# Kernel tuning notes

Hardware: AMD Instinct MI355X
Metric: run time of the kernel (lower is better)

Reference implementation:

```python
import jax, jax.numpy as jnp
import numpy as np

B, G, A, NC, NL = 64, 32, 25600, 2, 5
IOU_T, RATIO, FACE = 0.5, 3, 1
A_BOX, A_LMK, A_GAZE = 1.0, 0.5, 1.0
VAR_C, VAR_S = 0.1, 0.2  # SSD encode variances


def cxcywh_to_xyxy(b):
    return jnp.concatenate([b[..., :2] - b[..., 2:] / 2, b[..., :2] + b[..., 2:] / 2], -1)


def make_anchors():
    g = 160  # 160*160 = 25600 anchors
    c = (jnp.arange(g, dtype=jnp.float32) + 0.5) / g
    cy, cx = jnp.meshgrid(c, c, indexing='ij')
    wh = jnp.full((g * g, 2), 0.04, jnp.float32)
    return jnp.concatenate([cx.reshape(-1, 1), cy.reshape(-1, 1), wh], 1)  # [A,4] cxcywh


def setup_inputs() -> dict:
    key = jax.random.key(0)
    ks = jax.random.split(key, 8)
    cxy = jax.random.uniform(ks[0], (B, G, 2), minval=0.1, maxval=0.9)
    wh = jax.random.uniform(ks[1], (B, G, 2), minval=0.03, maxval=0.25)
    gt_boxes = jnp.concatenate([cxy - wh / 2, cxy + wh / 2], -1)  # xyxy in [0,1]
    return {
        'cls_logits': jax.random.normal(ks[2], (B, A, NC)),
        'box_preds': jax.random.normal(ks[3], (B, A, 4)),
        'lmk_preds': jax.random.normal(ks[4], (B, A, NL * 2)),
        'gaze_preds': jax.random.normal(ks[5], (B, A, 2)),
        'anchors': make_anchors(),
        'gt_boxes': gt_boxes,
        'gt_labels': jax.random.randint(ks[6], (B, G), 0, 2, jnp.int32),  # 0=pad, 1=face
        'gt_landmarks': jax.random.uniform(ks[7], (B, G, NL * 2)),
        'gt_gaze': jax.random.normal(jax.random.fold_in(key, 9), (B, G, 2)) * 0.3,
    }


def _smooth_l1(x):
    ax = jnp.abs(x)
    return jnp.where(ax < 1.0, 0.5 * ax * ax, ax - 0.5)


def _iou(gt, anc):  # [G,4],[A,4] xyxy -> [G,A]
    tl = jnp.maximum(gt[:, None, :2], anc[None, :, :2])
    br = jnp.minimum(gt[:, None, 2:], anc[None, :, 2:])
    inter = jnp.prod(jnp.clip(br - tl, 0.0), -1)
    ag = jnp.prod(gt[:, 2:] - gt[:, :2], -1)
    aa = jnp.prod(anc[:, 2:] - anc[:, :2], -1)
    return inter / (ag[:, None] + aa[None, :] - inter + 1e-9)


def _build_targets(anchors, gt_boxes, gt_labels, gt_landmarks, gt_gaze):
    anchors_xyxy = cxcywh_to_xyxy(anchors)
    dcxy, dwh = anchors[:, :2], anchors[:, 2:]

    def match(gt_b, lab, lmk, gz):
        valid = lab > 0
        iou = jnp.where(valid[:, None], _iou(gt_b, anchors_xyxy), -1.0)  # [G,A]
        # each valid GT claims its best anchor
        best_anchor_idx = jnp.where(valid, jnp.argmax(iou, 1), A)  # A -> dropped
        matches = jnp.full((A,), -1, jnp.int32).at[best_anchor_idx].set(
            jnp.arange(G, dtype=jnp.int32), mode='drop')
        # anchors above IoU threshold take their best GT
        best_gt_iou = iou.max(0)
        best_gt_idx = jnp.argmax(iou, 0).astype(jnp.int32)
        matches = jnp.where(best_gt_iou >= IOU_T, best_gt_idx, matches)
        pos = matches >= 0
        m = jnp.clip(matches, 0)
        cls = jnp.where(pos, lab[m], 0)
        g = gt_b[m]  # [A,4] xyxy
        gcxy = (g[:, :2] + g[:, 2:]) / 2
        gwh = g[:, 2:] - g[:, :2]
        off = jnp.concatenate([(gcxy - dcxy) / dwh / VAR_C,
                               jnp.log(jnp.clip(gwh / dwh, 1e-6)) / VAR_S], -1)
        off = jnp.where(pos[:, None], off, 0.0)
        face = (cls == FACE) & pos
        lm = lmk[m].reshape(A, NL, 2)
        lmo = ((lm - dcxy[:, None, :]) / dwh[:, None, :] / VAR_C).reshape(A, NL * 2)
        lmo = jnp.where(face[:, None], lmo, 0.0)
        gzt = jnp.where(face[:, None], gz[m], 0.0)
        return cls, off, lmo, gzt

    return jax.vmap(match)(gt_boxes, gt_labels, gt_landmarks, gt_gaze)


def reference(cls_logits, box_preds, lmk_preds, gaze_preds, anchors,
              gt_boxes, gt_labels, gt_landmarks, gt_gaze):
    cls_t, box_t, lmk_t, gaze_t = _build_targets(anchors, gt_boxes, gt_labels,
                                                 gt_landmarks, gt_gaze)
    pos = cls_t > 0  # [B,A]
    num_pos = jnp.maximum(pos.sum(1), 1)  # [B] int
    npos_f = num_pos.sum().astype(jnp.float32)

    logp = jax.nn.log_softmax(cls_logits, -1)
    cls_loss = -jnp.take_along_axis(logp, cls_t[..., None], -1)[..., 0]  # [B,A]
    pos_sum = jnp.where(pos, cls_loss, 0.0).sum()
    # hard negative mining: per-image top-k of negative CE losses
    neg_losses = jnp.where(pos, -jnp.inf, cls_loss)
    srt = jnp.sort(neg_losses, 1)[:, ::-1]
    num_neg = jnp.minimum((~pos).sum(1), RATIO * num_pos)  # [B]
    take = jnp.arange(A)[None, :] < num_neg[:, None]
    neg_sum = jnp.where(take, srt, 0.0).sum()
    total_cls = (pos_sum + neg_sum) / npos_f

    total_box = jnp.where(pos[..., None], _smooth_l1(box_preds - box_t), 0.0).sum() / npos_f

    face = (cls_t == FACE) & pos
    nface_f = jnp.maximum(face.sum(1), 1).sum().astype(jnp.float32)
    total_lmk = jnp.where(face[..., None], _smooth_l1(lmk_preds - lmk_t), 0.0).sum() / nface_f
    total_gaze = jnp.where(face[..., None], _smooth_l1(gaze_preds - gaze_t), 0.0).sum() / nface_f

    total = total_cls + A_BOX * total_box + A_LMK * total_lmk + A_GAZE * total_gaze
    return (total, total_cls, total_box, total_lmk, total_gaze)
```

## Files before the change

### kernel.cpp

```cpp
#include <hip/hip_runtime.h>
#include <stdint.h>

#define B 64
#define G 32
#define A 25600
#define NC 2
#define NL 5
#define IOU_T 0.5f
#define VAR_C 0.1f
#define VAR_S 0.2f

#define MSPLIT 50
#define MCH (A / MSPLIT)
#define PF 8

#define NB2 256
#define BSCALE2 20.0f
#define CANDCAP 8192
#define ST 512
#define NW (ST / 64)

__device__ __forceinline__ float sl1(float x) {
    float ax = fabsf(x);
    return ax < 1.0f ? 0.5f * ax * ax : ax - 0.5f;
}

__device__ __forceinline__ int vbin(float closs) {
    int bin = (int)(closs * BSCALE2);
    return bin < 0 ? 0 : (bin > NB2 - 1 ? NB2 - 1 : bin);
}

__global__ __launch_bounds__(256) void fused_kernel(
    const float* __restrict__ cls_logits, const float* __restrict__ box_preds,
    const float* __restrict__ lmk_preds, const float* __restrict__ gaze_preds,
    const float* __restrict__ anchors, const float* __restrict__ gt_boxes,
    const int* __restrict__ gt_labels, const float* __restrict__ gt_lmk,
    const float* __restrict__ gt_gaze, signed char* __restrict__ matches,
    unsigned long long* __restrict__ gsplit, unsigned* __restrict__ negkey,
    unsigned* __restrict__ bhist, float* __restrict__ psplit,
    unsigned* __restrict__ gdone)
{
    const int b = blockIdx.x, s = blockIdx.y, tid = threadIdx.x;
    const int lane = tid & 63, wave = tid >> 6;
    __shared__ float4 sbox[G];
    __shared__ int sgorig[G], sinv[G];
    __shared__ unsigned long long sbest[G];
    __shared__ int s_nv;
    __shared__ float sgb[G * 4], slmk[G * NL * 2], sgz[G * 2];
    __shared__ int slab[G];
    __shared__ unsigned lhist[4][NB2];
    __shared__ float wred[4][8];

    if (b == 0 && s == 0 && tid == 0) *gdone = 0u;

    if (tid < G) {
        sbest[tid] = 0ULL;
        int valid = gt_labels[b * G + tid] > 0;
        unsigned long long mask = __ballot(valid);
        int pfx = __popcll(mask & ((1ULL << tid) - 1ULL));
        sinv[tid] = valid ? pfx : -1;
        if (valid) {
            sbox[pfx] = *(const float4*)(gt_boxes + (b * G + tid) * 4);
            sgorig[pfx] = tid;
        }
        if (tid == 0) s_nv = (int)__popcll(mask);
    }
    for (int i = tid; i < G * 4; i += 256) sgb[i] = gt_boxes[b * G * 4 + i];
    for (int i = tid; i < G * NL * 2; i += 256) slmk[i] = gt_lmk[b * G * NL * 2 + i];
    for (int i = tid; i < G * 2; i += 256) sgz[i] = gt_gaze[b * G * 2 + i];
    if (tid < G) slab[tid] = gt_labels[b * G + tid];
    for (int i = tid; i < 4 * NB2; i += 256) ((unsigned*)lhist)[i] = 0u;
    __syncthreads();
    const int nv = s_nv;

    signed char* mrow = matches + (size_t)b * A;
    const int a0 = s * MCH;
    const int aL = a0 + tid, aH = aL + 256;

    float4 anL = *(const float4*)(anchors + aL * 4);
    float4 anH = *(const float4*)(anchors + aH * 4);
    float axL0 = anL.x - anL.z * 0.5f, ayL0 = anL.y - anL.w * 0.5f;
    float axL1 = anL.x + anL.z * 0.5f, ayL1 = anL.y + anL.w * 0.5f;
    float aaL = (axL1 - axL0) * (ayL1 - ayL0);
    float axH0 = anH.x - anH.z * 0.5f, ayH0 = anH.y - anH.w * 0.5f;
    float axH1 = anH.x + anH.z * 0.5f, ayH1 = anH.y + anH.w * 0.5f;
    float aaH = (axH1 - axH0) * (ayH1 - ayH0);

    float wx0 = fminf(axL0, axH0), wy0 = fminf(ayL0, ayH0);
    float wx1 = fmaxf(axL1, axH1), wy1 = fmaxf(ayL1, ayH1);
    #pragma unroll
    for (int off = 32; off > 0; off >>= 1) {
        wx0 = fminf(wx0, __shfl_down(wx0, off));
        wy0 = fminf(wy0, __shfl_down(wy0, off));
        wx1 = fmaxf(wx1, __shfl_down(wx1, off));
        wy1 = fmaxf(wy1, __shfl_down(wy1, off));
    }
    wx0 = __shfl(wx0, 0); wy0 = __shfl(wy0, 0);
    wx1 = __shfl(wx1, 0); wy1 = __shfl(wy1, 0);

    float bestL = -2.0f, bestH = -2.0f;
    int bciL = 0, bciH = 0;
    for (int ci = 0; ci < nv; ++ci) {
        float4 bb = sbox[ci];
        if (bb.x < wx1 && bb.z > wx0 && bb.y < wy1 && bb.w > wy0) {
            float area = (bb.z - bb.x) * (bb.w - bb.y);
            float iwL = fmaxf(fminf(bb.z, axL1) - fmaxf(bb.x, axL0), 0.0f);
            float ihL = fmaxf(fminf(bb.w, ayL1) - fmaxf(bb.y, ayL0), 0.0f);
            float interL = iwL * ihL;
            float iwH = fmaxf(fminf(bb.z, axH1) - fmaxf(bb.x, axH0), 0.0f);
            float ihH = fmaxf(fminf(bb.w, ayH1) - fmaxf(bb.y, ayH0), 0.0f);
            float interH = iwH * ihH;
            float iouL = 0.0f, iouH = 0.0f;
            if (__any(interL > 0.0f || interH > 0.0f)) {
                iouL = interL / (area + aaL - interL + 1e-9f);
                iouH = interH / (area + aaH - interH + 1e-9f);
                unsigned long long keyL =
                    ((unsigned long long)__float_as_uint(iouL) << 32) |
                    (unsigned)(0xFFFFFFFFu - (unsigned)aL);
                unsigned long long keyH =
                    ((unsigned long long)__float_as_uint(iouH) << 32) |
                    (unsigned)(0xFFFFFFFFu - (unsigned)aH);
                unsigned long long km = keyL > keyH ? keyL : keyH;
                #pragma unroll
                for (int off = 32; off > 0; off >>= 1) {
                    unsigned long long o = __shfl_down(km, off);
                    if (o > km) km = o;
                }
                if (lane == 0 && km > sbest[ci]) atomicMax(&sbest[ci], km);
            }
            if (iouL > bestL) { bestL = iouL; bciL = ci; }
            if (iouH > bestH) { bestH = iouH; bciH = ci; }
        } else {
            if (bestL < 0.0f) { bestL = 0.0f; bciL = ci; }
            if (bestH < 0.0f) { bestH = 0.0f; bciH = ci; }
        }
    }
    const int vL = (bestL >= IOU_T) ? sgorig[bciL] : -1;
    const int vH = (bestH >= IOU_T) ? sgorig[bciH] : -1;
    mrow[aL] = (signed char)vL;
    mrow[aH] = (signed char)vH;

    const float* lrow = cls_logits + (size_t)b * A * NC;
    unsigned* krow = negkey + (size_t)b * A;

    float pos_sum = 0, box_sum = 0, lmk_sum = 0, gaze_sum = 0;
    float pos_cnt = 0, face_cnt = 0;

    #pragma unroll
    for (int h = 0; h < 2; ++h) {
        const int a = h ? aH : aL;
        const int v = h ? vH : vL;
        const float4 an = h ? anH : anL;
        float2 xl = *(const float2*)(lrow + a * 2);
        float x0 = xl.x, x1 = xl.y;
        float mx = fmaxf(x0, x1);
        float lse = mx + logf(expf(x0 - mx) + expf(x1 - mx));
        unsigned key = 0;
        if (v < 0) {
            float closs = lse - x0;
            unsigned bits = __float_as_uint(closs);
            key = bits ^ ((bits & 0x80000000u) ? 0xFFFFFFFFu : 0x80000000u);
            atomicAdd(&lhist[wave][vbin(closs)], 1u);
        } else {
            int m = v;
            int lab = slab[m];
            float xc = (lab >= 1) ? x1 : x0;
            pos_sum += lse - xc;
            pos_cnt += 1.0f;
            float dcx = an.x, dcy = an.y, dw = an.z, dh = an.w;
            float bx0 = sgb[m * 4], by0 = sgb[m * 4 + 1];
            float bx1 = sgb[m * 4 + 2], by1 = sgb[m * 4 + 3];
            float gcx = (bx0 + bx1) * 0.5f, gcy = (by0 + by1) * 0.5f;
            float gw = bx1 - bx0, gh = by1 - by0;
            float off0 = ((gcx - dcx) / dw) / VAR_C;
            float off1 = ((gcy - dcy) / dh) / VAR_C;
            float off2 = logf(fmaxf(gw / dw, 1e-6f)) / VAR_S;
            float off3 = logf(fmaxf(gh / dh, 1e-6f)) / VAR_S;
            float4 bp = *(const float4*)(box_preds + ((size_t)b * A + a) * 4);
            box_sum += sl1(bp.x - off0) + sl1(bp.y - off1) +
                       sl1(bp.z - off2) + sl1(bp.w - off3);
            if (lab == 1) {
                face_cnt += 1.0f;
                const float* lp = lmk_preds + ((size_t)b * A + a) * (NL * 2);
                #pragma unroll
                for (int i = 0; i < NL; ++i) {
                    float tx = ((slmk[m * NL * 2 + 2 * i] - dcx) / dw) / VAR_C;
                    float ty = ((slmk[m * NL * 2 + 2 * i + 1] - dcy) / dh) / VAR_C;
                    lmk_sum += sl1(lp[2 * i] - tx) + sl1(lp[2 * i + 1] - ty);
                }
                const float* gp = gaze_preds + ((size_t)b * A + a) * 2;
                gaze_sum += sl1(gp[0] - sgz[m * 2]) + sl1(gp[1] - sgz[m * 2 + 1]);
            }
        }
        krow[a] = key;
    }

    #pragma unroll
    for (int off = 32; off > 0; off >>= 1) {
        pos_sum += __shfl_down(pos_sum, off);
        box_sum += __shfl_down(box_sum, off);
        lmk_sum += __shfl_down(lmk_sum, off);
        gaze_sum += __shfl_down(gaze_sum, off);
        pos_cnt += __shfl_down(pos_cnt, off);
        face_cnt += __shfl_down(face_cnt, off);
    }
    if (lane == 0) {
        wred[wave][0] = pos_sum; wred[wave][1] = box_sum;
        wred[wave][2] = lmk_sum; wred[wave][3] = gaze_sum;
        wred[wave][4] = pos_cnt; wred[wave][5] = face_cnt;
    }
    __syncthreads();
    if (tid < 6) {
        psplit[(b * MSPLIT + s) * PF + tid] =
            wred[0][tid] + wred[1][tid] + wred[2][tid] + wred[3][tid];
    }
    bhist[(b * MSPLIT + s) * NB2 + tid] =
        lhist[0][tid] + lhist[1][tid] + lhist[2][tid] + lhist[3][tid];
    if (tid < G) {
        int ci = sinv[tid];
        gsplit[((size_t)b * MSPLIT + s) * G + tid] = (ci >= 0) ? sbest[ci] : 0ULL;
    }
}

__global__ __launch_bounds__(ST) void select_kernel(
    const float* __restrict__ cls_logits, const float* __restrict__ box_preds,
    const float* __restrict__ lmk_preds, const float* __restrict__ gaze_preds,
    const float* __restrict__ anchors, const float* __restrict__ gt_boxes,
    const int* __restrict__ gt_labels, const float* __restrict__ gt_lmk,
    const float* __restrict__ gt_gaze, const signed char* __restrict__ matches,
    const unsigned long long* __restrict__ gsplit,
    unsigned* __restrict__ negkey, const unsigned* __restrict__ bhist,
    const float* __restrict__ psplit, unsigned* __restrict__ candbuf,
    float* __restrict__ partials, unsigned* __restrict__ gdone,
    float* __restrict__ out)
{
    const int b = blockIdx.x, tid = threadIdx.x;
    const int lane = tid & 63, wv = tid >> 6;
    __shared__ unsigned lhist[NB2];
    __shared__ unsigned whist[NW][256];
    __shared__ float accs[8];
    __shared__ float swred[NW];
    __shared__ int s_t, s_fin;
    __shared__ unsigned s_kk, s_candN, s_pfx, s_k2;

    unsigned* krow = negkey + (size_t)b * A;
    const uint4* krow4 = (const uint4*)krow;
    const float* lrow = cls_logits + (size_t)b * A * NC;
    unsigned* cand = candbuf + (size_t)b * CANDCAP;

    if (tid < 6) {
        float v = 0;
        for (int s2 = 0; s2 < MSPLIT; ++s2) v += psplit[(b * MSPLIT + s2) * PF + tid];
        accs[tid] = v;
    }
    if (tid < NB2) {
        unsigned v = 0;
        const unsigned* hb = bhist + (size_t)b * MSPLIT * NB2 + tid;
        for (int s2 = 0; s2 < MSPLIT; ++s2) v += hb[s2 * NB2];
        lhist[tid] = v;
    }
    if (tid == 0) s_candN = 0;
    __syncthreads();

    float f0 = 0, f1 = 0, f2 = 0, f3 = 0, f4 = 0, f5 = 0;
    int fbin = -1, fa = -1;
    if (tid < 32) {
        const int g = tid;
        int lab = gt_labels[b * G + g];
        unsigned long long kb = 0ULL;
        const unsigned long long* gs = gsplit + (size_t)b * MSPLIT * G + g;
        for (int s2 = 0; s2 < MSPLIT; ++s2) {
            unsigned long long v = gs[(size_t)s2 * G];
            if (v > kb) kb = v;
        }
        int a_c = -1;
        if (lab > 0 && kb != 0ULL) {
            unsigned a = 0xFFFFFFFFu - (unsigned)(kb & 0xFFFFFFFFu);
            if (matches[(size_t)b * A + a] < 0) a_c = (int)a;
        }
        bool win = a_c >= 0;
        for (int j = 0; j < 32; ++j) {
            int aj = __shfl(a_c, j);
            if (j > g && a_c >= 0 && aj == a_c) win = false;
        }
        if (win) {
            const int a = a_c;
            float2 xl = *(const float2*)(lrow + a * 2);
            float x0 = xl.x, x1 = xl.y;
            float mx = fmaxf(x0, x1);
            float lse = mx + logf(expf(x0 - mx) + expf(x1 - mx));
            float xc = (lab >= 1) ? x1 : x0;
            f0 = lse - xc; f4 = 1.0f;
            float4 an = *(const float4*)(anchors + a * 4);
            const float* gb = gt_boxes + (b * G + g) * 4;
            float bx0 = gb[0], by0 = gb[1], bx1 = gb[2], by1 = gb[3];
            float gcx = (bx0 + bx1) * 0.5f, gcy = (by0 + by1) * 0.5f;
            float gw = bx1 - bx0, gh = by1 - by0;
            float off0 = ((gcx - an.x) / an.z) / VAR_C;
            float off1 = ((gcy - an.y) / an.w) / VAR_C;
            float off2 = logf(fmaxf(gw / an.z, 1e-6f)) / VAR_S;
            float off3 = logf(fmaxf(gh / an.w, 1e-6f)) / VAR_S;
            float4 bp = *(const float4*)(box_preds + ((size_t)b * A + a) * 4);
            f1 = sl1(bp.x - off0) + sl1(bp.y - off1) +
                 sl1(bp.z - off2) + sl1(bp.w - off3);
            if (lab == 1) {
                f5 = 1.0f;
                const float* gl = gt_lmk + (b * G + g) * NL * 2;
                const float* lp = lmk_preds + ((size_t)b * A + a) * (NL * 2);
                #pragma unroll
                for (int i = 0; i < NL; ++i) {
                    float tx = ((gl[2 * i] - an.x) / an.z) / VAR_C;
                    float ty = ((gl[2 * i + 1] - an.y) / an.w) / VAR_C;
                    f2 += sl1(lp[2 * i] - tx) + sl1(lp[2 * i + 1] - ty);
                }
                const float* gz = gt_gaze + (b * G + g) * 2;
                const float* gp = gaze_preds + ((size_t)b * A + a) * 2;
                f3 = sl1(gp[0] - gz[0]) + sl1(gp[1] - gz[1]);
            }
            unsigned key = krow[a];
            float closs = __uint_as_float(key ^ 0x80000000u);
            fbin = vbin(closs); fa = a;
        }
    }
    if (tid < 64) {
        #pragma unroll
        for (int off = 16; off > 0; off >>= 1) {
            f0 += __shfl_down(f0, off); f1 += __shfl_down(f1, off);
            f2 += __shfl_down(f2, off); f3 += __shfl_down(f3, off);
            f4 += __shfl_down(f4, off); f5 += __shfl_down(f5, off);
        }
        if (tid == 0) {
            accs[0] += f0; accs[1] += f1; accs[2] += f2;
            accs[3] += f3; accs[4] += f4; accs[5] += f5;
        }
    }
    if (fbin >= 0) {
        atomicSub(&lhist[fbin], 1u);
        krow[fa] = 0u;
    }
    __syncthreads();

    unsigned pos_t = (unsigned)accs[4];
    unsigned face_t = (unsigned)accs[5];
    unsigned num_pos = pos_t > 1u ? pos_t : 1u;
    unsigned neg_cnt = (unsigned)A - pos_t;
    unsigned k = 3u * num_pos; if (neg_cnt < k) k = neg_cnt;

    if (tid < 64) {
        unsigned c[4]; unsigned csum = 0;
        #pragma unroll
        for (int j = 0; j < 4; ++j) { c[j] = lhist[tid * 4 + j]; csum += c[j]; }
        unsigned S = csum;
        #pragma unroll
        for (int off = 1; off < 64; off <<= 1) {
            unsigned t2 = __shfl_down(S, off);
            if (tid + off < 64) S += t2;
        }
        unsigned excl = S - csum;
        if (excl < k && excl + csum >= k) {
            unsigned cum = excl;
            #pragma unroll
            for (int j = 3; j >= 0; --j) {
                unsigned h = c[j];
                if (cum + h >= k) { s_t = tid * 4 + j; s_kk = k - cum; break; }
                cum += h;
            }
        }
    }
    __syncthreads();
    const int t = s_t;
    const unsigned kk_bin = s_kk;

    float nsum_top = 0.0f;
    for (int i = tid; i < A / 4; i += ST) {
        uint4 kv = krow4[i];
        #pragma unroll
        for (int j = 0; j < 4; ++j) {
            unsigned key = (&kv.x)[j];
            bool cp = false;
            if (key != 0u) {
                float closs = __uint_as_float(key ^ 0x80000000u);
                int bin = vbin(closs);
                if (bin > t) nsum_top += closs;
                else if (bin == t) cp = true;
            }
            unsigned long long m = __ballot(cp);
            if (m != 0ULL) {
                int leader = __ffsll((long long)m) - 1;
                unsigned base = 0u;
                if (lane == leader)
                    base = atomicAdd(&s_candN, (unsigned)__popcll(m));
                base = __shfl(base, leader);
                if (cp) {
                    unsigned idx = base + (unsigned)__popcll(m & ((1ULL << lane) - 1ULL));
                    if (idx < CANDCAP) cand[idx] = key;
                }
            }
        }
    }
    __syncthreads();
    const unsigned candN = s_candN;
    const bool fast = candN <= CANDCAP;

    unsigned pfx = 0, kk = kk_bin;
    for (int p = 0; p < 4; ++p) {
        for (int i = tid; i < NW * 256; i += ST) ((unsigned*)whist)[i] = 0u;
        __syncthreads();
        const int shift = 24 - 8 * p;
        if (fast) {
            for (unsigned i = tid; i < candN; i += ST) {
                unsigned key = cand[i];
                if (p == 0 || (key >> (shift + 8)) == pfx)
                    atomicAdd(&whist[wv][(key >> shift) & 0xFFu], 1u);
            }
        } else {
            for (int a = tid; a < A; a += ST) {
                unsigned key = krow[a];
                if (key != 0u && vbin(__uint_as_float(key ^ 0x80000000u)) == t &&
                    (p == 0 || (key >> (shift + 8)) == pfx))
                    atomicAdd(&whist[wv][(key >> shift) & 0xFFu], 1u);
            }
        }
        __syncthreads();
        if (tid < 64) {
            unsigned c[4]; unsigned csum = 0;
            #pragma unroll
            for (int j = 0; j < 4; ++j) {
                unsigned v = 0;
                #pragma unroll
                for (int w = 0; w < NW; ++w) v += whist[w][tid * 4 + j];
                c[j] = v; csum += v;
            }
            unsigned S = csum;
            #pragma unroll
            for (int off = 1; off < 64; off <<= 1) {
                unsigned t2 = __shfl_down(S, off);
                if (tid + off < 64) S += t2;
            }
            unsigned excl = S - csum;
            if (excl < kk && excl + csum >= kk) {
                unsigned cum = excl;
                #pragma unroll
                for (int j = 3; j >= 0; --j) {
                    unsigned h = c[j];
                    if (cum + h >= kk) {
                        s_pfx = (pfx << 8) | (unsigned)(tid * 4 + j);
                        s_k2 = kk - cum;
                        break;
                    }
                    cum += h;
                }
            }
        }
        __syncthreads();
        pfx = s_pfx; kk = s_k2;
    }
    const unsigned Tkey = pfx;
    const unsigned krem = kk;
    const float Tval = __uint_as_float(Tkey ^ 0x80000000u);

    float csum2 = 0.0f;
    if (fast) {
        for (unsigned i = tid; i < candN; i += ST) {
            unsigned key = cand[i];
            if (key > Tkey) csum2 += __uint_as_float(key ^ 0x80000000u);
        }
    } else {
        for (int a = tid; a < A; a += ST) {
            unsigned key = krow[a];
            if (key != 0u) {
                float closs = __uint_as_float(key ^ 0x80000000u);
                if (vbin(closs) == t && key > Tkey) csum2 += closs;
            }
        }
    }
    float tot = nsum_top + csum2;
    #pragma unroll
    for (int off = 32; off > 0; off >>= 1) tot += __shfl_down(tot, off);
    if (lane == 0) swred[wv] = tot;
    __syncthreads();
    if (tid == 0) {
        float r = 0;
        #pragma unroll
        for (int w = 0; w < NW; ++w) r += swred[w];
        float* pr = partials + b * PF;
        pr[0] = accs[0]; pr[1] = accs[1]; pr[2] = accs[2]; pr[3] = accs[3];
        pr[4] = r + (float)krem * Tval;
        pr[5] = (float)num_pos;
        pr[6] = (float)(face_t > 1u ? face_t : 1u);
        __threadfence();
        unsigned r2 = atomicAdd(gdone, 1u);
        s_fin = (r2 == B - 1);
    }
    __syncthreads();
    if (!s_fin) return;
    __threadfence();

    if (tid < 64) {
        int tt = tid;
        float ps = partials[tt * PF + 0], bs = partials[tt * PF + 1];
        float ls = partials[tt * PF + 2], gs = partials[tt * PF + 3];
        float ns = partials[tt * PF + 4], npos = partials[tt * PF + 5];
        float nf = partials[tt * PF + 6];
        #pragma unroll
        for (int o = 32; o > 0; o >>= 1) {
            ps += __shfl_down(ps, o); bs += __shfl_down(bs, o);
            ls += __shfl_down(ls, o); gs += __shfl_down(gs, o);
            ns += __shfl_down(ns, o); npos += __shfl_down(npos, o);
            nf += __shfl_down(nf, o);
        }
        if (tt == 0) {
            float tc = (ps + ns) / npos;
            float tb = bs / npos;
            float tl = ls / nf;
            float tg = gs / nf;
            out[0] = tc + 1.0f * tb + 0.5f * tl + 1.0f * tg;
            out[1] = tc; out[2] = tb; out[3] = tl; out[4] = tg;
        }
    }
}

extern "C" void kernel_launch(void* const* d_in, const int* in_sizes, int n_in,
                              void* d_out, int out_size, void* d_ws, size_t ws_size,
                              hipStream_t stream) {
    const float* cls_logits = (const float*)d_in[0];
    const float* box_preds  = (const float*)d_in[1];
    const float* lmk_preds  = (const float*)d_in[2];
    const float* gaze_preds = (const float*)d_in[3];
    const float* anchors    = (const float*)d_in[4];
    const float* gt_boxes   = (const float*)d_in[5];
    const int*   gt_labels  = (const int*)d_in[6];
    const float* gt_lmk     = (const float*)d_in[7];
    const float* gt_gaze    = (const float*)d_in[8];

    char* ws = (char*)d_ws;
    signed char* matches = (signed char*)ws;             ws += (size_t)B * A;
    unsigned long long* gsplit = (unsigned long long*)ws; ws += (size_t)B * MSPLIT * G * 8;
    unsigned* negkey = (unsigned*)ws;                    ws += (size_t)B * A * 4;
    unsigned* bhist = (unsigned*)ws;                     ws += (size_t)B * MSPLIT * NB2 * 4;
    unsigned* candbuf = (unsigned*)ws;                   ws += (size_t)B * CANDCAP * 4;
    float* psplit = (float*)ws;                          ws += (size_t)B * MSPLIT * PF * 4;
    float* partials = (float*)ws;                        ws += (size_t)B * PF * 4;
    unsigned* gdone = (unsigned*)ws;                     ws += 4;
    float* out = (float*)d_out;

    hipLaunchKernelGGL(fused_kernel, dim3(B, MSPLIT), dim3(256), 0, stream,
                       cls_logits, box_preds, lmk_preds, gaze_preds, anchors,
                       gt_boxes, gt_labels, gt_lmk, gt_gaze, matches, gsplit,
                       negkey, bhist, psplit, gdone);
    hipLaunchKernelGGL(select_kernel, dim3(B), dim3(ST), 0, stream,
                       cls_logits, box_preds, lmk_preds, gaze_preds, anchors,
                       gt_boxes, gt_labels, gt_lmk, gt_gaze, matches, gsplit,
                       negkey, bhist, psplit, candbuf, partials, gdone, out);
}
```

Baseline: 52.37 us.

## Drop matches buffer, recompute anchor IoU, parallelize split reductions in select

Removes the per-anchor matches byte array. The select kernel instead recomputes, for each GT's best anchor, the maximum IoU against all valid GTs. The serial per-thread loops over MSPLIT partial sums, histograms and gsplit maxima become wave-level shuffle reductions and shared-memory atomics spread across all threads. This cuts global writes in the first kernel and shortens the serial prologue of the per-image select kernel, at the cost of a small amount of redundant IoU math, one extra barrier and LDS atomics.

```diff
diff --git a/kernel.cpp b/kernel.cpp
--- a/kernel.cpp
+++ b/kernel.cpp
@@ -35,7 +35,7 @@
     const float* __restrict__ lmk_preds, const float* __restrict__ gaze_preds,
     const float* __restrict__ anchors, const float* __restrict__ gt_boxes,
     const int* __restrict__ gt_labels, const float* __restrict__ gt_lmk,
-    const float* __restrict__ gt_gaze, signed char* __restrict__ matches,
+    const float* __restrict__ gt_gaze,
     unsigned long long* __restrict__ gsplit, unsigned* __restrict__ negkey,
     unsigned* __restrict__ bhist, float* __restrict__ psplit,
     unsigned* __restrict__ gdone)
@@ -73,7 +73,6 @@
     __syncthreads();
     const int nv = s_nv;
 
-    signed char* mrow = matches + (size_t)b * A;
     const int a0 = s * MCH;
     const int aL = a0 + tid, aH = aL + 256;
 
@@ -137,8 +136,6 @@
     }
     const int vL = (bestL >= IOU_T) ? sgorig[bciL] : -1;
     const int vH = (bestH >= IOU_T) ? sgorig[bciH] : -1;
-    mrow[aL] = (signed char)vL;
-    mrow[aH] = (signed char)vH;
 
     const float* lrow = cls_logits + (size_t)b * A * NC;
     unsigned* krow = negkey + (size_t)b * A;
@@ -227,7 +224,7 @@
     const float* __restrict__ lmk_preds, const float* __restrict__ gaze_preds,
     const float* __restrict__ anchors, const float* __restrict__ gt_boxes,
     const int* __restrict__ gt_labels, const float* __restrict__ gt_lmk,
-    const float* __restrict__ gt_gaze, const signed char* __restrict__ matches,
+    const float* __restrict__ gt_gaze,
     const unsigned long long* __restrict__ gsplit,
     unsigned* __restrict__ negkey, const unsigned* __restrict__ bhist,
     const float* __restrict__ psplit, unsigned* __restrict__ candbuf,
@@ -238,6 +235,7 @@
     const int lane = tid & 63, wv = tid >> 6;
     __shared__ unsigned lhist[NB2];
     __shared__ unsigned whist[NW][256];
+    __shared__ unsigned long long skb[G];
     __shared__ float accs[8];
     __shared__ float swred[NW];
     __shared__ int s_t, s_fin;
@@ -248,18 +246,36 @@
     const float* lrow = cls_logits + (size_t)b * A * NC;
     unsigned* cand = candbuf + (size_t)b * CANDCAP;
 
-    if (tid < 6) {
-        float v = 0;
-        for (int s2 = 0; s2 < MSPLIT; ++s2) v += psplit[(b * MSPLIT + s2) * PF + tid];
-        accs[tid] = v;
-    }
-    if (tid < NB2) {
-        unsigned v = 0;
-        const unsigned* hb = bhist + (size_t)b * MSPLIT * NB2 + tid;
-        for (int s2 = 0; s2 < MSPLIT; ++s2) v += hb[s2 * NB2];
-        lhist[tid] = v;
-    }
+    if (wv < 6) {
+        float v = 0.0f;
+        if (lane < MSPLIT) v = psplit[(b * MSPLIT + lane) * PF + wv];
+        #pragma unroll
+        for (int off = 32; off > 0; off >>= 1) v += __shfl_down(v, off);
+        if (lane == 0) accs[wv] = v;
+    }
+    if (tid < NB2) lhist[tid] = 0u;
     if (tid == 0) s_candN = 0;
+    __syncthreads();
+    for (int i = tid; i < MSPLIT * NB2; i += ST) {
+        unsigned v = bhist[(size_t)b * MSPLIT * NB2 + i];
+        if (v) atomicAdd(&lhist[i & (NB2 - 1)], v);
+    }
+
+    {
+        const int g = tid >> 4, j = tid & 15;
+        unsigned long long kb = 0ULL;
+        const unsigned long long* gs = gsplit + (size_t)b * MSPLIT * G + g;
+        for (int s2 = j; s2 < MSPLIT; s2 += 16) {
+            unsigned long long v = gs[(size_t)s2 * G];
+            if (v > kb) kb = v;
+        }
+        #pragma unroll
+        for (int off = 8; off > 0; off >>= 1) {
+            unsigned long long o = __shfl_xor(kb, off);
+            if (o > kb) kb = o;
+        }
+        if (j == 0) skb[g] = kb;
+    }
     __syncthreads();
 
     float f0 = 0, f1 = 0, f2 = 0, f3 = 0, f4 = 0, f5 = 0;
@@ -267,16 +283,27 @@
     if (tid < 32) {
         const int g = tid;
         int lab = gt_labels[b * G + g];
-        unsigned long long kb = 0ULL;
-        const unsigned long long* gs = gsplit + (size_t)b * MSPLIT * G + g;
-        for (int s2 = 0; s2 < MSPLIT; ++s2) {
-            unsigned long long v = gs[(size_t)s2 * G];
-            if (v > kb) kb = v;
-        }
+        unsigned long long kb = skb[g];
         int a_c = -1;
         if (lab > 0 && kb != 0ULL) {
             unsigned a = 0xFFFFFFFFu - (unsigned)(kb & 0xFFFFFFFFu);
-            if (matches[(size_t)b * A + a] < 0) a_c = (int)a;
+            float4 an = *(const float4*)(anchors + a * 4);
+            float ax0 = an.x - an.z * 0.5f, ay0 = an.y - an.w * 0.5f;
+            float ax1 = an.x + an.z * 0.5f, ay1 = an.y + an.w * 0.5f;
+            float aa = (ax1 - ax0) * (ay1 - ay0);
+            float best = -2.0f;
+            for (int g2 = 0; g2 < G; ++g2) {
+                if (gt_labels[b * G + g2] <= 0) continue;
+                const float* gb2 = gt_boxes + (b * G + g2) * 4;
+                float bx = gb2[0], by = gb2[1], bz = gb2[2], bw = gb2[3];
+                float area = (bz - bx) * (bw - by);
+                float iw = fmaxf(fminf(bz, ax1) - fmaxf(bx, ax0), 0.0f);
+                float ih = fmaxf(fminf(bw, ay1) - fmaxf(by, ay0), 0.0f);
+                float inter = iw * ih;
+                float iou = inter / (area + aa - inter + 1e-9f);
+                if (iou > best) best = iou;
+            }
+            if (best < IOU_T) a_c = (int)a;
         }
         bool win = a_c >= 0;
         for (int j = 0; j < 32; ++j) {
@@ -322,6 +349,7 @@
             fbin = vbin(closs); fa = a;
         }
     }
+    __syncthreads();
     if (tid < 64) {
         #pragma unroll
         for (int off = 16; off > 0; off >>= 1) {
@@ -534,7 +562,6 @@
     const float* gt_gaze    = (const float*)d_in[8];
 
     char* ws = (char*)d_ws;
-    signed char* matches = (signed char*)ws;             ws += (size_t)B * A;
     unsigned long long* gsplit = (unsigned long long*)ws; ws += (size_t)B * MSPLIT * G * 8;
     unsigned* negkey = (unsigned*)ws;                    ws += (size_t)B * A * 4;
     unsigned* bhist = (unsigned*)ws;                     ws += (size_t)B * MSPLIT * NB2 * 4;
@@ -546,10 +573,10 @@
 
     hipLaunchKernelGGL(fused_kernel, dim3(B, MSPLIT), dim3(256), 0, stream,
                        cls_logits, box_preds, lmk_preds, gaze_preds, anchors,
-                       gt_boxes, gt_labels, gt_lmk, gt_gaze, matches, gsplit,
+                       gt_boxes, gt_labels, gt_lmk, gt_gaze, gsplit,
                        negkey, bhist, psplit, gdone);
     hipLaunchKernelGGL(select_kernel, dim3(B), dim3(ST), 0, stream,
                        cls_logits, box_preds, lmk_preds, gaze_preds, anchors,
-                       gt_boxes, gt_labels, gt_lmk, gt_gaze, matches, gsplit,
+                       gt_boxes, gt_labels, gt_lmk, gt_gaze, gsplit,
                        negkey, bhist, psplit, candbuf, partials, gdone, out);
 }
```

Result: slower. 57.78 us (+10.3%).
